# Performance work log

Measured on AMD Instinct MI355X. Metric: run time of the kernel, lower is better.

## Reference

```python
import jax, jax.numpy as jnp
import numpy as np

H = 32          # num attention heads
KVH = 8         # num key/value heads
D = 128         # head_dim
G = H // KVH    # num_key_value_groups
HID = 4096
EPS = 1e-5
SCALE = D ** -0.5


def rms_norm(x, w, eps=EPS):
    # x: [..., D]; computed in fp32 as in MllamaTextRMSNorm
    xf = x.astype(jnp.float32)
    var = jnp.mean(xf * xf, axis=-1, keepdims=True)
    return (w * (xf * jax.lax.rsqrt(var + eps)).astype(x.dtype))


def setup_inputs() -> dict:
    key = jax.random.key(0)
    ks = jax.random.split(key, 5)
    q_len, kv_len = 1024, 6404
    return {
        "hidden_states": jax.random.normal(ks[0], (q_len, HID), jnp.float32),
        "cross_attention_states": jax.random.normal(ks[1], (kv_len, HID), jnp.float32),
        "attention_mask": jnp.zeros((q_len, kv_len), jnp.float32),
        "w_qkv": jax.random.normal(ks[2], (HID, (H + 2 * KVH) * D), jnp.float32) * (HID ** -0.5),
        "w_o": jax.random.normal(ks[3], (H * D, HID), jnp.float32) * ((H * D) ** -0.5),
        "q_norm_w": jnp.ones((D,), jnp.float32),
        "k_norm_w": jnp.ones((D,), jnp.float32),
    }


def reference(hidden_states, cross_attention_states, attention_mask,
              w_qkv, w_o, q_norm_w, k_norm_w):
    q_len = hidden_states.shape[0]
    kv_len = cross_attention_states.shape[0]

    # QKV projections (decoder side only uses q; encoder side only k, v)
    qkv_dec = hidden_states @ w_qkv                       # [q_len, (H+2*KVH)*D]
    q = qkv_dec[:, : H * D]
    qkv_enc = cross_attention_states @ w_qkv              # [kv_len, (H+2*KVH)*D]
    k = qkv_enc[:, H * D: H * D + KVH * D]
    v = qkv_enc[:, H * D + KVH * D:]

    q = rms_norm(q.reshape(q_len, H, D), q_norm_w)        # [q_len, H, D]
    k = rms_norm(k.reshape(kv_len, KVH, D), k_norm_w)     # [kv_len, KVH, D]
    v = v.reshape(kv_len, KVH, D)

    # GQA layout: head h = kvh * G + g  (matches torch view(KVH, G, ...))
    q4 = q.transpose(1, 0, 2).reshape(KVH, G, q_len, D)   # [KVH, G, q_len, D]
    kt = k.transpose(1, 0, 2)                             # [KVH, kv_len, D]
    vt = v.transpose(1, 0, 2)                             # [KVH, kv_len, D]

    scores = jnp.einsum('kgqd,kld->kgql', q4, kt) * SCALE
    scores = scores + attention_mask[None, None, :, :]    # additive float mask
    probs = jax.nn.softmax(scores, axis=-1)
    out = jnp.einsum('kgql,kld->kgqd', probs, vt)         # [KVH, G, q_len, D]

    out = out.transpose(2, 0, 1, 3).reshape(q_len, H * D)
    return out @ w_o                                      # [q_len, HID]
```

## Files before the change

kernel.cpp:

```cpp
#include <hip/hip_runtime.h>

typedef unsigned short u16;
typedef unsigned int u32;
typedef __bf16 bf16x8 __attribute__((ext_vector_type(8)));
typedef float f32x4 __attribute__((ext_vector_type(4)));

#define HH 32
#define KVHH 8
#define DD 128
#define HID 4096
#define SCALE_Q 0.08838834764831845f

static __device__ __forceinline__ float bf2f(u32 u) { u <<= 16; return __builtin_bit_cast(float, u); }
static __device__ __forceinline__ u16 f2bf(float f) {
  u32 x = __builtin_bit_cast(u32, f);
  return (u16)((x + 0x7fffu + ((x >> 16) & 1u)) >> 16);
}
static __device__ __forceinline__ void gll16(const void* g, void* l) {
  __builtin_amdgcn_global_load_lds((const __attribute__((address_space(1))) void*)g,
                                   (__attribute__((address_space(3))) void*)l, 16, 0, 0);
}
static __device__ __forceinline__ f32x4 mfma16(bf16x8 a, bf16x8 b, f32x4 c) {
  return __builtin_amdgcn_mfma_f32_16x16x32_bf16(a, b, c, 0, 0, 0);
}

__global__ __launch_bounds__(256) void cvt_f32_bf16(const float* __restrict__ in, u16* __restrict__ out, size_t n4) {
  size_t i = (size_t)blockIdx.x * blockDim.x + threadIdx.x;
  size_t stride = (size_t)gridDim.x * blockDim.x;
  for (; i < n4; i += stride) {
    float4 v = ((const float4*)in)[i];
    ushort4 o;
    o.x = f2bf(v.x); o.y = f2bf(v.y); o.z = f2bf(v.z); o.w = f2bf(v.w);
    ((ushort4*)out)[i] = o;
  }
}

__global__ __launch_bounds__(256) void transpose_cvt(const float* __restrict__ in, u16* __restrict__ out, int K, int N) {
  __shared__ float t[64][68];
  int k0 = blockIdx.x * 64, n0 = blockIdx.y * 64;
  int tid = threadIdx.x;
  int r = tid >> 4, c4 = (tid & 15) << 2;
#pragma unroll
  for (int i = 0; i < 4; ++i) {
    float4 v = *(const float4*)(in + (size_t)(k0 + r + i * 16) * N + n0 + c4);
    t[r + i * 16][c4 + 0] = v.x; t[r + i * 16][c4 + 1] = v.y;
    t[r + i * 16][c4 + 2] = v.z; t[r + i * 16][c4 + 3] = v.w;
  }
  __syncthreads();
#pragma unroll
  for (int i = 0; i < 4; ++i) {
    int rr = r + i * 16;
    ushort4 o;
    o.x = f2bf(t[c4 + 0][rr]); o.y = f2bf(t[c4 + 1][rr]);
    o.z = f2bf(t[c4 + 2][rr]); o.w = f2bf(t[c4 + 3][rr]);
    *(ushort4*)(out + (size_t)(n0 + rr) * K + k0 + c4) = o;
  }
}

__global__ __launch_bounds__(256) void transpose_bf(const u16* __restrict__ in, u16* __restrict__ out,
                                                    int ldin, int colOff, int ldout) {
  __shared__ u16 t[64][72];
  int m0 = blockIdx.x * 64, n0 = blockIdx.y * 64;
  int tid = threadIdx.x;
  int r = tid >> 4, c4 = (tid & 15) << 2;
#pragma unroll
  for (int i = 0; i < 4; ++i) {
    ushort4 v = *(const ushort4*)(in + (size_t)(m0 + r + i * 16) * ldin + colOff + n0 + c4);
    t[r + i * 16][c4 + 0] = v.x; t[r + i * 16][c4 + 1] = v.y;
    t[r + i * 16][c4 + 2] = v.z; t[r + i * 16][c4 + 3] = v.w;
  }
  __syncthreads();
#pragma unroll
  for (int i = 0; i < 4; ++i) {
    int rr = r + i * 16;
    ushort4 o;
    o.x = t[c4 + 0][rr]; o.y = t[c4 + 1][rr]; o.z = t[c4 + 2][rr]; o.w = t[c4 + 3][rr];
    *(ushort4*)(out + (size_t)(n0 + rr) * ldout + m0 + c4) = o;
  }
}

__global__ __launch_bounds__(256) void rmsnorm_kernel(u16* __restrict__ x, const float* __restrict__ w,
                                                      int totalRows, int heads, int ld, float scale) {
  int gw = blockIdx.x * 4 + (threadIdx.x >> 6);
  if (gw >= totalRows) return;
  int lane = threadIdx.x & 63;
  int row = gw / heads, h = gw - row * heads;
  u16* p = x + (size_t)row * ld + h * 128 + lane * 2;
  u32 u = *(const u32*)p;
  float a = bf2f(u & 0xffffu), b = bf2f(u >> 16);
  float ss = a * a + b * b;
#pragma unroll
  for (int o = 1; o < 64; o <<= 1) ss += __shfl_xor(ss, o);
  float inv = rsqrtf(ss * (1.0f / 128.0f) + 1e-5f) * scale;
  float oa = a * inv * w[lane * 2], ob = b * inv * w[lane * 2 + 1];
  *(u32*)p = (u32)f2bf(oa) | ((u32)f2bf(ob) << 16);
}

template <int STOREF32, int CLAMP>
__global__ __launch_bounds__(256, 2) void gemm_bt(const u16* __restrict__ A, const u16* __restrict__ B,
                                                  void* __restrict__ C, int N, int K, int Mclamp, int Mstore) {
  __shared__ __align__(16) char As[16384];
  __shared__ __align__(16) char Bs[16384];
  const int tid = threadIdx.x, lane = tid & 63, wave = tid >> 6;
  const int wr = wave >> 1, wc = wave & 1;
  const int l15 = lane & 15, lg = lane >> 4;
  const int m0 = blockIdx.x * 128, n0 = blockIdx.y * 128;
  f32x4 acc[4][4] = {};
  const int kIters = K >> 6;
  int srow[4], scb[4], sbase[4];
#pragma unroll
  for (int q = 0; q < 4; ++q) {
    sbase[q] = (wave * 4 + q) * 1024;
    int off = sbase[q] + lane * 16;
    srow[q] = off >> 7;
    scb[q] = (off & 127) ^ ((srow[q] & 7) << 4);
  }
  for (int kt = 0; kt < kIters; ++kt) {
    __syncthreads();
#pragma unroll
    for (int q = 0; q < 4; ++q) {
      int ar = m0 + srow[q];
      if (CLAMP) ar = min(ar, Mclamp - 1);
      gll16(A + (size_t)ar * K + kt * 64 + (scb[q] >> 1), As + sbase[q]);
      gll16(B + (size_t)(n0 + srow[q]) * K + kt * 64 + (scb[q] >> 1), Bs + sbase[q]);
    }
    __syncthreads();
#pragma unroll
    for (int kk = 0; kk < 2; ++kk) {
      bf16x8 af[4], bfr[4];
#pragma unroll
      for (int mt = 0; mt < 4; ++mt) {
        int rr = wr * 64 + mt * 16 + l15;
        int cb = ((kk * 32 + lg * 8) * 2) ^ ((rr & 7) << 4);
        af[mt] = *(const bf16x8*)(As + rr * 128 + cb);
      }
#pragma unroll
      for (int nt = 0; nt < 4; ++nt) {
        int rr = wc * 64 + nt * 16 + l15;
        int cb = ((kk * 32 + lg * 8) * 2) ^ ((rr & 7) << 4);
        bfr[nt] = *(const bf16x8*)(Bs + rr * 128 + cb);
      }
#pragma unroll
      for (int mt = 0; mt < 4; ++mt)
#pragma unroll
        for (int nt = 0; nt < 4; ++nt)
          acc[mt][nt] = mfma16(af[mt], bfr[nt], acc[mt][nt]);
    }
  }
#pragma unroll
  for (int mt = 0; mt < 4; ++mt) {
#pragma unroll
    for (int nt = 0; nt < 4; ++nt) {
      int cc = n0 + wc * 64 + nt * 16 + l15;
#pragma unroll
      for (int j = 0; j < 4; ++j) {
        int cr = m0 + wr * 64 + mt * 16 + lg * 4 + j;
        if (CLAMP && cr >= Mstore) continue;
        if (STOREF32) ((float*)C)[(size_t)cr * N + cc] = acc[mt][nt][j];
        else ((u16*)C)[(size_t)cr * N + cc] = f2bf(acc[mt][nt][j]);
      }
    }
  }
}

__global__ __launch_bounds__(256, 2) void attn_kernel(const u16* __restrict__ q, const u16* __restrict__ kv,
                                                      const u16* __restrict__ vT, const float* __restrict__ mask,
                                                      float* __restrict__ pO, float2* __restrict__ ml,
                                                      int kv_len, int kv_tiles, int kvp, int tiles_per_split) {
  __shared__ __align__(16) char Ks[2][16384];
  __shared__ __align__(16) char Vs[2][16384];
  __shared__ __align__(16) u16 Ps[4][16][72];
  const int tid = threadIdx.x, lane = tid & 63, wave = tid >> 6;
  const int l15 = lane & 15, lg = lane >> 4;
  const int h = blockIdx.y, kvh = h >> 2;
  const int qb = blockIdx.x * 64 + wave * 16;
  const int split = blockIdx.z;
  const int t0 = split * tiles_per_split;
  const int t1 = min(t0 + tiles_per_split, kv_tiles);

  bf16x8 qa[4];
  {
    const u16* qp = q + (size_t)(qb + l15) * 4096 + h * 128 + lg * 8;
    qa[0] = *(const bf16x8*)(qp);
    qa[1] = *(const bf16x8*)(qp + 32);
    qa[2] = *(const bf16x8*)(qp + 64);
    qa[3] = *(const bf16x8*)(qp + 96);
  }
  int base[4], krow[4], kcb[4], vrow[4], vcb[4];
#pragma unroll
  for (int qq = 0; qq < 4; ++qq) {
    base[qq] = (wave * 4 + qq) * 1024;
    int off = base[qq] + lane * 16;
    krow[qq] = off >> 8; kcb[qq] = (off & 255) ^ ((krow[qq] & 15) << 4);
    vrow[qq] = off >> 7; vcb[qq] = (off & 127) ^ ((vrow[qq] & 7) << 4);
  }
#define STAGE(T, B)                                                                             \
  {                                                                                             \
    const int kt = (T) * 64;                                                                    \
    _Pragma("unroll") for (int qq = 0; qq < 4; ++qq) {                                          \
      gll16(kv + (size_t)(kt + krow[qq]) * 2048 + kvh * 128 + (kcb[qq] >> 1), Ks[B] + base[qq]);\
      gll16(vT + (size_t)(kvh * 128 + vrow[qq]) * kvp + kt + (vcb[qq] >> 1), Vs[B] + base[qq]); \
    }                                                                                           \
  }

  f32x4 o[8] = {};
  float m_r[4], l_r[4];
#pragma unroll
  for (int j = 0; j < 4; ++j) { m_r[j] = -1e30f; l_r[j] = 0.0f; }

  STAGE(t0, 0);
  __syncthreads();

  for (int t = t0; t < t1; ++t) {
    const int cur = (t - t0) & 1;
    const int kt0 = t * 64;
    float mf[4][4];
#pragma unroll
    for (int c = 0; c < 4; ++c) {
      int kvi = kt0 + c * 16 + l15;
      const float* mp = mask + (size_t)(qb + lg * 4) * kv_len + min(kvi, kv_len - 1);
#pragma unroll
      for (int j = 0; j < 4; ++j) mf[c][j] = mp[(size_t)j * kv_len];
    }
    if (t + 1 < t1) STAGE(t + 1, cur ^ 1);
    f32x4 s[4] = {};
#pragma unroll
    for (int kk = 0; kk < 4; ++kk)
#pragma unroll
      for (int c = 0; c < 4; ++c) {
        int rr = c * 16 + l15;
        int cb = ((kk * 32 + lg * 8) * 2) ^ ((rr & 15) << 4);
        bf16x8 b = *(const bf16x8*)(Ks[cur] + rr * 256 + cb);
        s[c] = mfma16(qa[kk], b, s[c]);
      }
#pragma unroll
    for (int c = 0; c < 4; ++c) {
      int kvi = kt0 + c * 16 + l15;
      bool valid = kvi < kv_len;
#pragma unroll
      for (int j = 0; j < 4; ++j)
        s[c][j] = valid ? s[c][j] + mf[c][j] : -1e30f;
    }
#pragma unroll
    for (int j = 0; j < 4; ++j) {
      float tm = fmaxf(fmaxf(s[0][j], s[1][j]), fmaxf(s[2][j], s[3][j]));
      tm = fmaxf(tm, __shfl_xor(tm, 1));
      tm = fmaxf(tm, __shfl_xor(tm, 2));
      tm = fmaxf(tm, __shfl_xor(tm, 4));
      tm = fmaxf(tm, __shfl_xor(tm, 8));
      float mn = fmaxf(m_r[j], tm);
      float alpha = __expf(m_r[j] - mn);
      m_r[j] = mn;
      float rs = 0.0f;
#pragma unroll
      for (int c = 0; c < 4; ++c) {
        float p = __expf(s[c][j] - mn);
        s[c][j] = p;
        rs += p;
      }
      rs += __shfl_xor(rs, 1);
      rs += __shfl_xor(rs, 2);
      rs += __shfl_xor(rs, 4);
      rs += __shfl_xor(rs, 8);
      l_r[j] = l_r[j] * alpha + rs;
#pragma unroll
      for (int dt = 0; dt < 8; ++dt) o[dt][j] *= alpha;
#pragma unroll
      for (int c = 0; c < 4; ++c) Ps[wave][lg * 4 + j][c * 16 + l15] = f2bf(s[c][j]);
    }
#pragma unroll
    for (int kk2 = 0; kk2 < 2; ++kk2) {
      bf16x8 a = *(const bf16x8*)&Ps[wave][l15][kk2 * 32 + lg * 8];
#pragma unroll
      for (int dt = 0; dt < 8; ++dt) {
        int rr = dt * 16 + l15;
        int cb = ((kk2 * 32 + lg * 8) * 2) ^ ((rr & 7) << 4);
        bf16x8 b = *(const bf16x8*)(Vs[cur] + rr * 128 + cb);
        o[dt] = mfma16(a, b, o[dt]);
      }
    }
    __syncthreads();
  }
#pragma unroll
  for (int j = 0; j < 4; ++j) {
    int row = qb + lg * 4 + j;
    float* op = pO + (size_t)split * 4194304 + (size_t)row * 4096 + h * 128 + l15;
#pragma unroll
    for (int dt = 0; dt < 8; ++dt) op[dt * 16] = o[dt][j];
    if (l15 == 0) ml[(size_t)split * 32768 + row * 32 + h] = make_float2(m_r[j], l_r[j]);
  }
#undef STAGE
}

__global__ __launch_bounds__(256) void attn_combine(const float* __restrict__ pO, const float2* __restrict__ ml,
                                                    u16* __restrict__ out) {
  int gw = blockIdx.x * 4 + (threadIdx.x >> 6);
  int lane = threadIdx.x & 63;
  int row = gw >> 5, h = gw & 31;
  float2 A = ml[row * 32 + h];
  float2 B = ml[32768 + row * 32 + h];
  float M = fmaxf(A.x, B.x);
  float e0 = __expf(A.x - M), e1 = __expf(B.x - M);
  float inv = 1.0f / (A.y * e0 + B.y * e1);
  const float* p0 = pO + (size_t)row * 4096 + h * 128 + lane * 2;
  const float* p1 = p0 + 4194304;
  float2 v0 = *(const float2*)p0, v1 = *(const float2*)p1;
  float o0 = (v0.x * e0 + v1.x * e1) * inv;
  float o1 = (v0.y * e0 + v1.y * e1) * inv;
  u16* op = out + (size_t)row * 4096 + h * 128 + lane * 2;
  *(u32*)op = (u32)f2bf(o0) | ((u32)f2bf(o1) << 16);
}

extern "C" void kernel_launch(void* const* d_in, const int* in_sizes, int n_in,
                              void* d_out, int out_size, void* d_ws, size_t ws_size,
                              hipStream_t stream) {
  const float* hidden = (const float*)d_in[0];
  const float* cross = (const float*)d_in[1];
  const float* mask = (const float*)d_in[2];
  const float* w_qkv = (const float*)d_in[3];
  const float* w_o = (const float*)d_in[4];
  const float* q_norm_w = (const float*)d_in[5];
  const float* k_norm_w = (const float*)d_in[6];
  const int q_len = in_sizes[0] / HID;
  const int kv_len = in_sizes[1] / HID;
  const int kvp = ((kv_len + 127) / 128) * 128;
  const int kv_tiles = (kv_len + 63) / 64;
  const int tps = (kv_tiles + 1) / 2;

  char* w = (char*)d_ws;
  u16* hB = (u16*)w;    w += (size_t)q_len * HID * 2;
  u16* cB = (u16*)w;    w += (size_t)kv_len * HID * 2;
  u16* wqkvT = (u16*)w; w += (size_t)6144 * 4096 * 2;
  u16* woT = (u16*)w;   w += (size_t)4096 * 4096 * 2;
  u16* qrw = (u16*)w;   w += (size_t)q_len * 4096 * 2;
  u16* kvr = (u16*)w;   w += (size_t)kvp * 2048 * 2;
  u16* vT = (u16*)w;    w += (size_t)1024 * kvp * 2;
  u16* aO = (u16*)w;    w += (size_t)q_len * 4096 * 2;
  float* pO = (float*)wqkvT;
  float2* mlp = (float2*)((char*)wqkvT + 2u * 16777216u);

  cvt_f32_bf16<<<1024, 256, 0, stream>>>(hidden, hB, (size_t)q_len * HID / 4);
  cvt_f32_bf16<<<2048, 256, 0, stream>>>(cross, cB, (size_t)kv_len * HID / 4);
  transpose_cvt<<<dim3(64, 96), 256, 0, stream>>>(w_qkv, wqkvT, 4096, 6144);
  transpose_cvt<<<dim3(64, 64), 256, 0, stream>>>(w_o, woT, 4096, 4096);

  gemm_bt<0, 0><<<dim3(q_len / 128, 32), 256, 0, stream>>>(hB, wqkvT, qrw, 4096, 4096, 0, 0);
  rmsnorm_kernel<<<(q_len * 32 + 3) / 4, 256, 0, stream>>>(qrw, q_norm_w, q_len * 32, 32, 4096, SCALE_Q);

  gemm_bt<0, 1><<<dim3(kvp / 128, 16), 256, 0, stream>>>(cB, wqkvT + (size_t)4096 * 4096, kvr, 2048, 4096, kv_len, kvp);
  rmsnorm_kernel<<<(kvp * 8 + 3) / 4, 256, 0, stream>>>(kvr, k_norm_w, kvp * 8, 8, 2048, 1.0f);
  transpose_bf<<<dim3(kvp / 64, 16), 256, 0, stream>>>(kvr, vT, 2048, 1024, kvp);

  attn_kernel<<<dim3(q_len / 64, HH, 2), 256, 0, stream>>>(qrw, kvr, vT, mask, pO, mlp, kv_len, kv_tiles, kvp, tps);
  attn_combine<<<(q_len * HH) / 4, 256, 0, stream>>>(pO, mlp, aO);

  gemm_bt<1, 0><<<dim3(q_len / 128, 32), 256, 0, stream>>>(aO, woT, d_out, 4096, 4096, 0, 0);
}
```

Baseline: 927.1 us.

## Double-buffer GEMM tiles, widen attention blocks, add lazy softmax rescale

```diff
diff --git a/kernel.cpp b/kernel.cpp
--- a/kernel.cpp
+++ b/kernel.cpp
@@ -99,8 +99,8 @@
 template <int STOREF32, int CLAMP>
 __global__ __launch_bounds__(256, 2) void gemm_bt(const u16* __restrict__ A, const u16* __restrict__ B,
                                                   void* __restrict__ C, int N, int K, int Mclamp, int Mstore) {
-  __shared__ __align__(16) char As[16384];
-  __shared__ __align__(16) char Bs[16384];
+  __shared__ __align__(16) char As[2][16384];
+  __shared__ __align__(16) char Bs[2][16384];
   const int tid = threadIdx.x, lane = tid & 63, wave = tid >> 6;
   const int wr = wave >> 1, wc = wave & 1;
   const int l15 = lane & 15, lg = lane >> 4;
@@ -115,16 +115,20 @@
     srow[q] = off >> 7;
     scb[q] = (off & 127) ^ ((srow[q] & 7) << 4);
   }
+#define GSTAGE(KT, BUF)                                                              \
+  {                                                                                  \
+    _Pragma("unroll") for (int q2 = 0; q2 < 4; ++q2) {                               \
+      int ar = m0 + srow[q2];                                                        \
+      if (CLAMP) ar = min(ar, Mclamp - 1);                                           \
+      gll16(A + (size_t)ar * K + (KT) * 64 + (scb[q2] >> 1), As[BUF] + sbase[q2]);   \
+      gll16(B + (size_t)(n0 + srow[q2]) * K + (KT) * 64 + (scb[q2] >> 1), Bs[BUF] + sbase[q2]); \
+    }                                                                                \
+  }
+  GSTAGE(0, 0);
+  __syncthreads();
   for (int kt = 0; kt < kIters; ++kt) {
-    __syncthreads();
-#pragma unroll
-    for (int q = 0; q < 4; ++q) {
-      int ar = m0 + srow[q];
-      if (CLAMP) ar = min(ar, Mclamp - 1);
-      gll16(A + (size_t)ar * K + kt * 64 + (scb[q] >> 1), As + sbase[q]);
-      gll16(B + (size_t)(n0 + srow[q]) * K + kt * 64 + (scb[q] >> 1), Bs + sbase[q]);
-    }
-    __syncthreads();
+    const int cur = kt & 1;
+    if (kt + 1 < kIters) GSTAGE(kt + 1, cur ^ 1);
 #pragma unroll
     for (int kk = 0; kk < 2; ++kk) {
       bf16x8 af[4], bfr[4];
@@ -132,13 +136,13 @@
       for (int mt = 0; mt < 4; ++mt) {
         int rr = wr * 64 + mt * 16 + l15;
         int cb = ((kk * 32 + lg * 8) * 2) ^ ((rr & 7) << 4);
-        af[mt] = *(const bf16x8*)(As + rr * 128 + cb);
+        af[mt] = *(const bf16x8*)(As[cur] + rr * 128 + cb);
       }
 #pragma unroll
       for (int nt = 0; nt < 4; ++nt) {
         int rr = wc * 64 + nt * 16 + l15;
         int cb = ((kk * 32 + lg * 8) * 2) ^ ((rr & 7) << 4);
-        bfr[nt] = *(const bf16x8*)(Bs + rr * 128 + cb);
+        bfr[nt] = *(const bf16x8*)(Bs[cur] + rr * 128 + cb);
       }
 #pragma unroll
       for (int mt = 0; mt < 4; ++mt)
@@ -146,7 +150,9 @@
         for (int nt = 0; nt < 4; ++nt)
           acc[mt][nt] = mfma16(af[mt], bfr[nt], acc[mt][nt]);
     }
-  }
+    __syncthreads();
+  }
+#undef GSTAGE
 #pragma unroll
   for (int mt = 0; mt < 4; ++mt) {
 #pragma unroll
@@ -163,17 +169,17 @@
   }
 }
 
-__global__ __launch_bounds__(256, 2) void attn_kernel(const u16* __restrict__ q, const u16* __restrict__ kv,
+__global__ __launch_bounds__(512, 4) void attn_kernel(const u16* __restrict__ q, const u16* __restrict__ kv,
                                                       const u16* __restrict__ vT, const float* __restrict__ mask,
                                                       float* __restrict__ pO, float2* __restrict__ ml,
                                                       int kv_len, int kv_tiles, int kvp, int tiles_per_split) {
   __shared__ __align__(16) char Ks[2][16384];
   __shared__ __align__(16) char Vs[2][16384];
-  __shared__ __align__(16) u16 Ps[4][16][72];
+  __shared__ __align__(16) char PsB[16384];
   const int tid = threadIdx.x, lane = tid & 63, wave = tid >> 6;
   const int l15 = lane & 15, lg = lane >> 4;
   const int h = blockIdx.y, kvh = h >> 2;
-  const int qb = blockIdx.x * 64 + wave * 16;
+  const int qb = blockIdx.x * 128 + wave * 16;
   const int split = blockIdx.z;
   const int t0 = split * tiles_per_split;
   const int t1 = min(t0 + tiles_per_split, kv_tiles);
@@ -186,10 +192,10 @@
     qa[2] = *(const bf16x8*)(qp + 64);
     qa[3] = *(const bf16x8*)(qp + 96);
   }
-  int base[4], krow[4], kcb[4], vrow[4], vcb[4];
-#pragma unroll
-  for (int qq = 0; qq < 4; ++qq) {
-    base[qq] = (wave * 4 + qq) * 1024;
+  int base[2], krow[2], kcb[2], vrow[2], vcb[2];
+#pragma unroll
+  for (int qq = 0; qq < 2; ++qq) {
+    base[qq] = (wave * 2 + qq) * 1024;
     int off = base[qq] + lane * 16;
     krow[qq] = off >> 8; kcb[qq] = (off & 255) ^ ((krow[qq] & 15) << 4);
     vrow[qq] = off >> 7; vcb[qq] = (off & 127) ^ ((vrow[qq] & 7) << 4);
@@ -197,7 +203,7 @@
 #define STAGE(T, B)                                                                             \
   {                                                                                             \
     const int kt = (T) * 64;                                                                    \
-    _Pragma("unroll") for (int qq = 0; qq < 4; ++qq) {                                          \
+    _Pragma("unroll") for (int qq = 0; qq < 2; ++qq) {                                          \
       gll16(kv + (size_t)(kt + krow[qq]) * 2048 + kvh * 128 + (kcb[qq] >> 1), Ks[B] + base[qq]);\
       gll16(vT + (size_t)(kvh * 128 + vrow[qq]) * kvp + kt + (vcb[qq] >> 1), Vs[B] + base[qq]); \
     }                                                                                           \
@@ -248,13 +254,18 @@
       tm = fmaxf(tm, __shfl_xor(tm, 2));
       tm = fmaxf(tm, __shfl_xor(tm, 4));
       tm = fmaxf(tm, __shfl_xor(tm, 8));
-      float mn = fmaxf(m_r[j], tm);
-      float alpha = __expf(m_r[j] - mn);
-      m_r[j] = mn;
+      if (__any(tm > m_r[j] + 8.0f)) {
+        float mn = fmaxf(m_r[j], tm);
+        float alpha = __expf(m_r[j] - mn);
+        m_r[j] = mn;
+        l_r[j] *= alpha;
+#pragma unroll
+        for (int dt = 0; dt < 8; ++dt) o[dt][j] *= alpha;
+      }
       float rs = 0.0f;
 #pragma unroll
       for (int c = 0; c < 4; ++c) {
-        float p = __expf(s[c][j] - mn);
+        float p = __expf(s[c][j] - m_r[j]);
         s[c][j] = p;
         rs += p;
       }
@@ -262,15 +273,17 @@
       rs += __shfl_xor(rs, 2);
       rs += __shfl_xor(rs, 4);
       rs += __shfl_xor(rs, 8);
-      l_r[j] = l_r[j] * alpha + rs;
-#pragma unroll
-      for (int dt = 0; dt < 8; ++dt) o[dt][j] *= alpha;
-#pragma unroll
-      for (int c = 0; c < 4; ++c) Ps[wave][lg * 4 + j][c * 16 + l15] = f2bf(s[c][j]);
+      l_r[j] += rs;
+      const int r = lg * 4 + j;
+#pragma unroll
+      for (int c = 0; c < 4; ++c) {
+        int cb = ((c * 16 + l15) * 2) ^ ((r & 7) << 4);
+        *(u16*)(PsB + wave * 2048 + r * 128 + cb) = f2bf(s[c][j]);
+      }
     }
 #pragma unroll
     for (int kk2 = 0; kk2 < 2; ++kk2) {
-      bf16x8 a = *(const bf16x8*)&Ps[wave][l15][kk2 * 32 + lg * 8];
+      bf16x8 a = *(const bf16x8*)(PsB + wave * 2048 + l15 * 128 + ((kk2 * 64 + lg * 16) ^ ((l15 & 7) << 4)));
 #pragma unroll
       for (int dt = 0; dt < 8; ++dt) {
         int rr = dt * 16 + l15;
@@ -351,7 +364,7 @@
   rmsnorm_kernel<<<(kvp * 8 + 3) / 4, 256, 0, stream>>>(kvr, k_norm_w, kvp * 8, 8, 2048, 1.0f);
   transpose_bf<<<dim3(kvp / 64, 16), 256, 0, stream>>>(kvr, vT, 2048, 1024, kvp);
 
-  attn_kernel<<<dim3(q_len / 64, HH, 2), 256, 0, stream>>>(qrw, kvr, vT, mask, pO, mlp, kv_len, kv_tiles, kvp, tps);
+  attn_kernel<<<dim3(q_len / 128, HH, 2), 512, 0, stream>>>(qrw, kvr, vT, mask, pO, mlp, kv_len, kv_tiles, kvp, tps);
   attn_combine<<<(q_len * HH) / 4, 256, 0, stream>>>(pO, mlp, aO);
 
   gemm_bt<1, 0><<<dim3(q_len / 128, 32), 256, 0, stream>>>(aO, woT, d_out, 4096, 4096, 0, 0);
```

Measured after the change: 1.019 ms. 1.1x slower.
